# Optimization experiments

Hardware: AMD Instinct MI355X
Metric: run time of the kernel (lower is better)

Reference implementation:

```python
import jax, jax.numpy as jnp
import numpy as np

N = 100000
F = 128
H = 16
C = 40
E = 3200000


def _gcn_norm(edge_index, num_nodes):
    # add self-loops, compute symmetric normalization (PyG GCNConv default)
    loops = jnp.arange(num_nodes, dtype=edge_index.dtype)
    src = jnp.concatenate([edge_index[0], loops])
    dst = jnp.concatenate([edge_index[1], loops])
    ones = jnp.ones(src.shape[0], dtype=jnp.float32)
    deg = jax.ops.segment_sum(ones, dst, num_segments=num_nodes)
    dinv = jnp.where(deg > 0, jax.lax.rsqrt(deg), 0.0)
    norm = dinv[src] * dinv[dst]  # [E+N]
    return src, dst, norm


def _gcn_conv(x, W, b, src, dst, norm, num_nodes):
    h = x @ W                                   # [N, out] transform first (PyG order)
    msg = h[src] * norm[:, None]                # gather + scale
    agg = jax.ops.segment_sum(msg, dst, num_segments=num_nodes)  # scatter-add
    return agg + b


def setup_inputs() -> dict:
    key = jax.random.key(0)
    k = jax.random.split(key, 6)
    x = jax.random.normal(k[0], (N, F), dtype=jnp.float32)
    edge_index = jax.random.randint(k[1], (2, E), 0, N, dtype=jnp.int64)
    W1 = jax.random.normal(k[2], (F, H), dtype=jnp.float32) / np.sqrt(F)
    b1 = jnp.zeros((H,), dtype=jnp.float32)
    W2 = jax.random.normal(k[3], (H, C), dtype=jnp.float32) / np.sqrt(H)
    b2 = jnp.zeros((C,), dtype=jnp.float32)
    return {"x": x, "edge_index": edge_index, "W1": W1, "b1": b1, "W2": W2, "b2": b2}


def reference(x, edge_index, W1, b1, W2, b2):
    src, dst, norm = _gcn_norm(edge_index, N)
    h = _gcn_conv(x, W1, b1, src, dst, norm, N)
    h = jax.nn.relu(h)
    out = _gcn_conv(h, W2, b2, src, dst, norm, N)
    return out
```

## Files before the change

kernel.cpp:

```cpp
#include <hip/hip_runtime.h>
#include <hip/hip_fp16.h>


#define N_NODES 100000
#define F_IN    128
#define H_MID   16
#define C_OUT   40
#define N_EDGES 3200000

#define EC      8192
#define EBLK    391
#define NBUK    782
#define M_HIST  (NBUK * EBLK)
#define NPART   598
#define SRC_MASK 0x1FFFF
#define NSTRIDE 100352
#define CAP_H   5632


__global__ void __launch_bounds__(1024) k_hist(
    const int* __restrict__ dst, int* __restrict__ hist) {
    __shared__ int h[NBUK];
    int t = threadIdx.x, blk = blockIdx.x;
    for (int i = t; i < NBUK; i += 1024) h[i] = 0;
    __syncthreads();
#pragma unroll
    for (int i = 0; i < EC / 1024; ++i) {
        int e = blk * EC + i * 1024 + t;
        if (e < N_EDGES) atomicAdd(&h[__builtin_nontemporal_load(dst + e) >> 7], 1);
    }
    __syncthreads();
    for (int b = t; b < NBUK; b += 1024) hist[b * EBLK + blk] = h[b];
}

__global__ void __launch_bounds__(512) k_scanA(int* __restrict__ hist,
                                               int* __restrict__ part) {
    __shared__ int s[512];
    int t = threadIdx.x;
    int i = blockIdx.x * 512 + t;
    int v = (i < M_HIST) ? hist[i] : 0;
    s[t] = v;
    __syncthreads();
    for (int off = 1; off < 512; off <<= 1) {
        int x = (t >= off) ? s[t - off] : 0;
        __syncthreads();
        s[t] += x;
        __syncthreads();
    }
    if (i < M_HIST) hist[i] = s[t] - v;
    if (t == 511) part[blockIdx.x] = s[511];
}

__global__ void __launch_bounds__(1024) k_scanB(int* __restrict__ part) {
    __shared__ int s[1024];
    int t = threadIdx.x;
    int v = (t < NPART) ? part[t] : 0;
    s[t] = v;
    __syncthreads();
    for (int off = 1; off < 1024; off <<= 1) {
        int x = (t >= off) ? s[t - off] : 0;
        __syncthreads();
        s[t] += x;
        __syncthreads();
    }
    if (t < NPART) part[t] = s[t] - v;
}

__global__ void __launch_bounds__(1024) k_part(
    const int* __restrict__ src, const int* __restrict__ dst,
    const int* __restrict__ hist, const int* __restrict__ part,
    int* __restrict__ eb) {
    __shared__ int cnt[NBUK];
    __shared__ int scn[1024];
    __shared__ int dlt[NBUK];
    __shared__ int cr[NBUK];
    __shared__ int sval[EC];
    __shared__ int spos[EC];
    int t = threadIdx.x, blk = blockIdx.x;
    for (int b = t; b < NBUK; b += 1024) cnt[b] = 0;
    __syncthreads();
    int e0 = blk * EC;
    int d[8], s[8], bk[8];
    bool val[8];
#pragma unroll
    for (int k = 0; k < 8; ++k) {
        int e = e0 + k * 1024 + t;
        val[k] = (e < N_EDGES);
        d[k] = val[k] ? __builtin_nontemporal_load(dst + e) : 0;
        s[k] = val[k] ? __builtin_nontemporal_load(src + e) : 0;
        bk[k] = d[k] >> 7;
    }
#pragma unroll
    for (int k = 0; k < 8; ++k)
        if (val[k]) atomicAdd(&cnt[bk[k]], 1);
    __syncthreads();
    scn[t] = (t < NBUK) ? cnt[t] : 0;
    __syncthreads();
    for (int off = 1; off < 1024; off <<= 1) {
        int x = (t >= off) ? scn[t - off] : 0;
        __syncthreads();
        scn[t] += x;
        __syncthreads();
    }
    for (int b = t; b < NBUK; b += 1024) {
        int idx = b * EBLK + blk;
        int gb = hist[idx] + part[idx >> 9];
        int lb = scn[b] - cnt[b];
        dlt[b] = gb - lb;
        cr[b] = lb;
    }
    __syncthreads();
#pragma unroll
    for (int k = 0; k < 8; ++k) {
        if (val[k]) {
            int lr = atomicAdd(&cr[bk[k]], 1);
            sval[lr] = ((d[k] & 127) << 17) | s[k];
            spos[lr] = lr + dlt[bk[k]];
        }
    }
    __syncthreads();
    int n = (e0 + EC <= N_EDGES) ? EC : (N_EDGES - e0);
    for (int i = t; i < n; i += 1024)
        eb[spos[i]] = sval[i];
}

__global__ void __launch_bounds__(512) k_degrp(
    const int* __restrict__ hist, const int* __restrict__ part,
    const int* __restrict__ eb, int* __restrict__ rp,
    float* __restrict__ dinv) {
    __shared__ int deg[128], scn[128];
    int b = blockIdx.x, t = threadIdx.x;
    int i0 = b * EBLK;
    int bb = hist[i0] + part[i0 >> 9];
    int bn = (b + 1 < NBUK) ? (hist[i0 + EBLK] + part[(i0 + EBLK) >> 9]) : N_EDGES;
    int ecnt = bn - bb;
    if (t < 128) deg[t] = 0;
    __syncthreads();
    for (int i = t; i < ecnt; i += 512)
        atomicAdd(&deg[__builtin_nontemporal_load(eb + bb + i) >> 17], 1);
    __syncthreads();
    if (t < 128) scn[t] = deg[t];
    __syncthreads();
    for (int off = 1; off < 128; off <<= 1) {
        int x = (t < 128 && t >= off) ? scn[t - off] : 0;
        __syncthreads();
        if (t < 128) scn[t] += x;
        __syncthreads();
    }
    if (t < 128) {
        int ex = scn[t] - deg[t];
        int node = b * 128 + t;
        rp[node] = bb + ex;
        dinv[node] = rsqrtf(1.0f + (float)deg[t]);
    }
}


typedef float f4 __attribute__((ext_vector_type(4)));

__global__ void __launch_bounds__(256) k_gemm1(
    const float* __restrict__ x, const float* __restrict__ W1,
    const float* __restrict__ dinv, __half* __restrict__ h1p) {
    __shared__ float w[F_IN * H_MID];
    __shared__ float xs[16 * 132];
    int t = threadIdx.x;
    for (int i = t; i < F_IN * H_MID; i += 256) w[i] = W1[i];
    int tile = blockIdx.x;
    const f4* xg = (const f4*)(x + (size_t)tile * 16 * F_IN);
    f4* xs4 = (f4*)xs;
    for (int i = t; i < 512; i += 256) {
        int r = i >> 5, c4 = i & 31;
        xs4[r * 33 + c4] = __builtin_nontemporal_load(xg + r * 32 + c4);
    }
    __syncthreads();
    int node = t >> 4, j = t & 15;
    const float* xr = xs + node * 132;
    float acc = 0.f;
#pragma unroll 8
    for (int k = 0; k < F_IN; ++k) acc += xr[k] * w[k * H_MID + j];
    int g = tile * 16 + node;
    h1p[(size_t)g * H_MID + j] = __float2half(acc * dinv[g]);
}

__global__ void __launch_bounds__(1024) k_csrg1(
    const int* __restrict__ hist, const int* __restrict__ part,
    const int* __restrict__ eb, const int* __restrict__ rp,
    const float* __restrict__ dinv, const __half* __restrict__ h1p,
    const float* __restrict__ b1, __half* __restrict__ r1p) {
    __shared__ int base[129];
    __shared__ int cw[128];
    __shared__ int esl[CAP_H];
    int b = blockIdx.x, t = threadIdx.x;
    int i0 = b * EBLK;
    int bb = hist[i0] + part[i0 >> 9];
    int bn = (b + 1 < NBUK) ? (hist[i0 + EBLK] + part[(i0 + EBLK) >> 9]) : N_EDGES;
    int ecnt = bn - bb;
    int n0 = b * 128;
    if (t < 128) {
        int lb = rp[n0 + t] - bb;
        base[t] = lb;
        cw[t] = lb;
    }
    if (t == 128) base[128] = ecnt;
    __syncthreads();
    int g = t >> 4, j = t & 15;
    if (ecnt <= CAP_H) {
        for (int i = t; i < ecnt; i += 1024) {
            int v = __builtin_nontemporal_load(eb + bb + i);
            int r = atomicAdd(&cw[v >> 17], 1);
            esl[r] = v & SRC_MASK;
        }
        __syncthreads();
        for (int nd = g; nd < 128; nd += 64) {
            int node = n0 + nd;
            if (node >= N_NODES) continue;
            float dv = dinv[node];
            int beg = base[nd], end = base[nd + 1];
            float acc = __half2float(h1p[(size_t)node * H_MID + j]);
            int e = beg;
            for (; e + 8 <= end; e += 8) {
                int s0 = esl[e],     s1 = esl[e + 1], s2 = esl[e + 2], s3 = esl[e + 3];
                int s4 = esl[e + 4], s5 = esl[e + 5], s6 = esl[e + 6], s7 = esl[e + 7];
                acc += __half2float(h1p[(size_t)s0 * H_MID + j])
                     + __half2float(h1p[(size_t)s1 * H_MID + j])
                     + __half2float(h1p[(size_t)s2 * H_MID + j])
                     + __half2float(h1p[(size_t)s3 * H_MID + j])
                     + __half2float(h1p[(size_t)s4 * H_MID + j])
                     + __half2float(h1p[(size_t)s5 * H_MID + j])
                     + __half2float(h1p[(size_t)s6 * H_MID + j])
                     + __half2float(h1p[(size_t)s7 * H_MID + j]);
            }
            for (; e < end; ++e) acc += __half2float(h1p[(size_t)esl[e] * H_MID + j]);
            float a = dv * acc;
            unsigned short o = __half_as_ushort(__float2half(fmaxf(a + b1[j], 0.f) * dv));
            __builtin_nontemporal_store(o, (unsigned short*)(r1p + (size_t)node * H_MID + j));
        }
    } else {
        for (int nd = g; nd < 128; nd += 64) {
            int node = n0 + nd;
            if (node >= N_NODES) continue;
            float dv = dinv[node];
            float acc = __half2float(h1p[(size_t)node * H_MID + j]);
            for (int i = 0; i < ecnt; ++i) {
                int v = eb[bb + i];
                if ((v >> 17) == nd)
                    acc += __half2float(h1p[(size_t)(v & SRC_MASK) * H_MID + j]);
            }
            float a = dv * acc;
            unsigned short o = __half_as_ushort(__float2half(fmaxf(a + b1[j], 0.f) * dv));
            __builtin_nontemporal_store(o, (unsigned short*)(r1p + (size_t)node * H_MID + j));
        }
    }
}

__global__ void __launch_bounds__(1024) k_csrg2(
    const int* __restrict__ hist, const int* __restrict__ part,
    const int* __restrict__ eb, const int* __restrict__ rp,
    const float* __restrict__ dinv, const __half* __restrict__ r1p,
    const float* __restrict__ W2, const float* __restrict__ b2,
    float* __restrict__ out) {
    __shared__ int base[129];
    __shared__ int cw[128];
    __shared__ int esl[CAP_H];
    __shared__ float a2[128 * 17];
    __shared__ float w2[H_MID * C_OUT];
    __shared__ float b2l[C_OUT];
    int b = blockIdx.x, t = threadIdx.x;
    int i0 = b * EBLK;
    int bb = hist[i0] + part[i0 >> 9];
    int bn = (b + 1 < NBUK) ? (hist[i0 + EBLK] + part[(i0 + EBLK) >> 9]) : N_EDGES;
    int ecnt = bn - bb;
    int n0 = b * 128;
    if (t < H_MID * C_OUT) w2[t] = W2[t];
    if (t >= 1024 - C_OUT) b2l[t - (1024 - C_OUT)] = b2[t - (1024 - C_OUT)];
    if (t < 128) {
        int lb = rp[n0 + t] - bb;
        base[t] = lb;
        cw[t] = lb;
    }
    if (t == 128) base[128] = ecnt;
    __syncthreads();
    int g = t >> 4, j = t & 15;
    if (ecnt <= CAP_H) {
        for (int i = t; i < ecnt; i += 1024) {
            int v = __builtin_nontemporal_load(eb + bb + i);
            int r = atomicAdd(&cw[v >> 17], 1);
            esl[r] = v & SRC_MASK;
        }
        __syncthreads();
        for (int nd = g; nd < 128; nd += 64) {
            int node = n0 + nd;
            float dv = (node < N_NODES) ? dinv[node] : 0.f;
            int beg = base[nd], end = base[nd + 1];
            float acc = (node < N_NODES) ? __half2float(r1p[(size_t)node * H_MID + j]) : 0.f;
            int e = beg;
            for (; e + 8 <= end; e += 8) {
                int s0 = esl[e],     s1 = esl[e + 1], s2 = esl[e + 2], s3 = esl[e + 3];
                int s4 = esl[e + 4], s5 = esl[e + 5], s6 = esl[e + 6], s7 = esl[e + 7];
                acc += __half2float(r1p[(size_t)s0 * H_MID + j])
                     + __half2float(r1p[(size_t)s1 * H_MID + j])
                     + __half2float(r1p[(size_t)s2 * H_MID + j])
                     + __half2float(r1p[(size_t)s3 * H_MID + j])
                     + __half2float(r1p[(size_t)s4 * H_MID + j])
                     + __half2float(r1p[(size_t)s5 * H_MID + j])
                     + __half2float(r1p[(size_t)s6 * H_MID + j])
                     + __half2float(r1p[(size_t)s7 * H_MID + j]);
            }
            for (; e < end; ++e) acc += __half2float(r1p[(size_t)esl[e] * H_MID + j]);
            a2[nd * 17 + j] = dv * acc;
        }
    } else {
        for (int nd = g; nd < 128; nd += 64) {
            int node = n0 + nd;
            float dv = (node < N_NODES) ? dinv[node] : 0.f;
            float acc = (node < N_NODES) ? __half2float(r1p[(size_t)node * H_MID + j]) : 0.f;
            for (int i = 0; i < ecnt; ++i) {
                int v = eb[bb + i];
                if ((v >> 17) == nd)
                    acc += __half2float(r1p[(size_t)(v & SRC_MASK) * H_MID + j]);
            }
            a2[nd * 17 + j] = dv * acc;
        }
    }
    __syncthreads();
    for (int idx = t; idx < 128 * C_OUT; idx += 1024) {
        int nd = idx / C_OUT, c = idx - nd * C_OUT;
        int node = n0 + nd;
        if (node < N_NODES) {
            float s = b2l[c];
#pragma unroll
            for (int jj = 0; jj < H_MID; ++jj) s += a2[nd * 17 + jj] * w2[jj * C_OUT + c];
            __builtin_nontemporal_store(s, &out[(size_t)node * C_OUT + c]);
        }
    }
}

extern "C" void kernel_launch(void* const* d_in, const int* in_sizes, int n_in,
                              void* d_out, int out_size, void* d_ws, size_t ws_size,
                              hipStream_t stream) {
    const float* x  = (const float*)d_in[0];
    const int*   ei = (const int*)d_in[1];
    const float* W1 = (const float*)d_in[2];
    const float* b1 = (const float*)d_in[3];
    const float* W2 = (const float*)d_in[4];
    const float* b2 = (const float*)d_in[5];
    float* out = (float*)d_out;

    const int* src = ei;
    const int* dst = ei + N_EDGES;

    int* rp     = (int*)d_ws;
    float* dinv = (float*)(rp + NSTRIDE);
    __half* h1p = (__half*)(dinv + NSTRIDE);
    __half* r1p = h1p + (size_t)NSTRIDE * H_MID;
    int* eb     = (int*)(r1p + (size_t)NSTRIDE * H_MID);
    int* hist   = eb + N_EDGES;
    int* part   = hist + 306176;

    k_hist <<<EBLK, 1024, 0, stream>>>(dst, hist);
    k_scanA<<<NPART, 512, 0, stream>>>(hist, part);
    k_scanB<<<1, 1024, 0, stream>>>(part);
    k_part <<<EBLK, 1024, 0, stream>>>(src, dst, hist, part, eb);
    k_degrp<<<NBUK, 512, 0, stream>>>(hist, part, eb, rp, dinv);
    k_gemm1<<<N_NODES / 16, 256, 0, stream>>>(x, W1, dinv, h1p);
    k_csrg1<<<NBUK, 1024, 0, stream>>>(hist, part, eb, rp, dinv, h1p, b1, r1p);
    k_csrg2<<<NBUK, 1024, 0, stream>>>(hist, part, eb, rp, dinv, r1p, W2, b2, out);
}
```

Before: 228.5 us.

## Fuse CSR build stages into one cooperative kernel with grid syncs

Replaces the five separate kernels (histogram, two scans, partition, degree/rowptr) with a single cooperative kernel that uses grid-wide syncs between phases. Edge chunks grow to 12800 per block so 250 blocks cover all edges, and each block keeps its dst/src values in registers and its bucket counts in shared memory across phases, so the partition step no longer re-reads edges from global memory. The aim is to remove launch gaps and the redundant reloads. In exchange it relies on all 250 blocks of 1024 threads, with about 100KB of shared memory each, being co-resident, and grid.sync has its own cost.

New measurement: 364.7 us. 1.6x slower.

```diff
diff --git a/kernel.cpp b/kernel.cpp
--- a/kernel.cpp
+++ b/kernel.cpp
@@ -1,5 +1,6 @@
 #include <hip/hip_runtime.h>
 #include <hip/hip_fp16.h>
+#include <hip/hip_cooperative_groups.h>
 
 
 #define N_NODES 100000
@@ -8,150 +9,136 @@
 #define C_OUT   40
 #define N_EDGES 3200000
 
-#define EC      8192
-#define EBLK    391
+#define EC      12800
+#define EBLK    250
+#define KPT     13
 #define NBUK    782
 #define M_HIST  (NBUK * EBLK)
-#define NPART   598
+#define NSEG    191
 #define SRC_MASK 0x1FFFF
 #define NSTRIDE 100352
 #define CAP_H   5632
 
-
-__global__ void __launch_bounds__(1024) k_hist(
-    const int* __restrict__ dst, int* __restrict__ hist) {
-    __shared__ int h[NBUK];
-    int t = threadIdx.x, blk = blockIdx.x;
-    for (int i = t; i < NBUK; i += 1024) h[i] = 0;
-    __syncthreads();
-#pragma unroll
-    for (int i = 0; i < EC / 1024; ++i) {
-        int e = blk * EC + i * 1024 + t;
-        if (e < N_EDGES) atomicAdd(&h[__builtin_nontemporal_load(dst + e) >> 7], 1);
-    }
-    __syncthreads();
-    for (int b = t; b < NBUK; b += 1024) hist[b * EBLK + blk] = h[b];
-}
-
-__global__ void __launch_bounds__(512) k_scanA(int* __restrict__ hist,
-                                               int* __restrict__ part) {
-    __shared__ int s[512];
-    int t = threadIdx.x;
-    int i = blockIdx.x * 512 + t;
-    int v = (i < M_HIST) ? hist[i] : 0;
-    s[t] = v;
-    __syncthreads();
-    for (int off = 1; off < 512; off <<= 1) {
-        int x = (t >= off) ? s[t - off] : 0;
-        __syncthreads();
-        s[t] += x;
-        __syncthreads();
-    }
-    if (i < M_HIST) hist[i] = s[t] - v;
-    if (t == 511) part[blockIdx.x] = s[511];
-}
-
-__global__ void __launch_bounds__(1024) k_scanB(int* __restrict__ part) {
-    __shared__ int s[1024];
-    int t = threadIdx.x;
-    int v = (t < NPART) ? part[t] : 0;
-    s[t] = v;
-    __syncthreads();
-    for (int off = 1; off < 1024; off <<= 1) {
-        int x = (t >= off) ? s[t - off] : 0;
-        __syncthreads();
-        s[t] += x;
-        __syncthreads();
-    }
-    if (t < NPART) part[t] = s[t] - v;
-}
-
-__global__ void __launch_bounds__(1024) k_part(
+namespace cg = cooperative_groups;
+
+
+__global__ void __launch_bounds__(1024) k_build(
     const int* __restrict__ src, const int* __restrict__ dst,
-    const int* __restrict__ hist, const int* __restrict__ part,
-    int* __restrict__ eb) {
+    int* __restrict__ hist, int* __restrict__ part, int* __restrict__ eb,
+    int* __restrict__ rp, float* __restrict__ dinv) {
     __shared__ int cnt[NBUK];
-    __shared__ int scn[1024];
     __shared__ int dlt[NBUK];
     __shared__ int cr[NBUK];
+    __shared__ int lscn[1024];
     __shared__ int sval[EC];
     __shared__ int spos[EC];
+    cg::grid_group grid = cg::this_grid();
     int t = threadIdx.x, blk = blockIdx.x;
+    int e0 = blk * EC;
+
     for (int b = t; b < NBUK; b += 1024) cnt[b] = 0;
     __syncthreads();
-    int e0 = blk * EC;
-    int d[8], s[8], bk[8];
-    bool val[8];
+    int d[KPT], s[KPT];
 #pragma unroll
-    for (int k = 0; k < 8; ++k) {
-        int e = e0 + k * 1024 + t;
-        val[k] = (e < N_EDGES);
-        d[k] = val[k] ? __builtin_nontemporal_load(dst + e) : 0;
-        s[k] = val[k] ? __builtin_nontemporal_load(src + e) : 0;
-        bk[k] = d[k] >> 7;
+    for (int k = 0; k < KPT; ++k) {
+        int off = k * 1024 + t;
+        if (off < EC) {
+            d[k] = __builtin_nontemporal_load(dst + e0 + off);
+            s[k] = __builtin_nontemporal_load(src + e0 + off);
+        } else { d[k] = 0; s[k] = 0; }
     }
 #pragma unroll
-    for (int k = 0; k < 8; ++k)
-        if (val[k]) atomicAdd(&cnt[bk[k]], 1);
-    __syncthreads();
-    scn[t] = (t < NBUK) ? cnt[t] : 0;
+    for (int k = 0; k < KPT; ++k)
+        if (k * 1024 + t < EC) atomicAdd(&cnt[d[k] >> 7], 1);
+    __syncthreads();
+    for (int b = t; b < NBUK; b += 1024) hist[b * EBLK + blk] = cnt[b];
+    grid.sync();
+
+    if (blk < NSEG) {
+        int i = blk * 1024 + t;
+        int v = (i < M_HIST) ? hist[i] : 0;
+        lscn[t] = v;
+        __syncthreads();
+        for (int off = 1; off < 1024; off <<= 1) {
+            int x = (t >= off) ? lscn[t - off] : 0;
+            __syncthreads();
+            lscn[t] += x;
+            __syncthreads();
+        }
+        if (i < M_HIST) hist[i] = lscn[t] - v;
+        if (t == 1023) part[blk] = lscn[1023];
+    }
+    grid.sync();
+
+    if (blk == 0) {
+        int v = (t < NSEG) ? part[t] : 0;
+        lscn[t] = v;
+        __syncthreads();
+        for (int off = 1; off < 1024; off <<= 1) {
+            int x = (t >= off) ? lscn[t - off] : 0;
+            __syncthreads();
+            lscn[t] += x;
+            __syncthreads();
+        }
+        if (t < NSEG) part[t] = lscn[t] - v;
+    }
+    grid.sync();
+
+    lscn[t] = (t < NBUK) ? cnt[t] : 0;
     __syncthreads();
     for (int off = 1; off < 1024; off <<= 1) {
-        int x = (t >= off) ? scn[t - off] : 0;
-        __syncthreads();
-        scn[t] += x;
+        int x = (t >= off) ? lscn[t - off] : 0;
+        __syncthreads();
+        lscn[t] += x;
         __syncthreads();
     }
     for (int b = t; b < NBUK; b += 1024) {
         int idx = b * EBLK + blk;
-        int gb = hist[idx] + part[idx >> 9];
-        int lb = scn[b] - cnt[b];
+        int gb = hist[idx] + part[idx >> 10];
+        int lb = lscn[b] - cnt[b];
         dlt[b] = gb - lb;
         cr[b] = lb;
     }
     __syncthreads();
 #pragma unroll
-    for (int k = 0; k < 8; ++k) {
-        if (val[k]) {
-            int lr = atomicAdd(&cr[bk[k]], 1);
+    for (int k = 0; k < KPT; ++k) {
+        if (k * 1024 + t < EC) {
+            int bk = d[k] >> 7;
+            int lr = atomicAdd(&cr[bk], 1);
             sval[lr] = ((d[k] & 127) << 17) | s[k];
-            spos[lr] = lr + dlt[bk[k]];
-        }
-    }
-    __syncthreads();
-    int n = (e0 + EC <= N_EDGES) ? EC : (N_EDGES - e0);
-    for (int i = t; i < n; i += 1024)
+            spos[lr] = lr + dlt[bk];
+        }
+    }
+    __syncthreads();
+    for (int i = t; i < EC; i += 1024)
         eb[spos[i]] = sval[i];
-}
-
-__global__ void __launch_bounds__(512) k_degrp(
-    const int* __restrict__ hist, const int* __restrict__ part,
-    const int* __restrict__ eb, int* __restrict__ rp,
-    float* __restrict__ dinv) {
-    __shared__ int deg[128], scn[128];
-    int b = blockIdx.x, t = threadIdx.x;
-    int i0 = b * EBLK;
-    int bb = hist[i0] + part[i0 >> 9];
-    int bn = (b + 1 < NBUK) ? (hist[i0 + EBLK] + part[(i0 + EBLK) >> 9]) : N_EDGES;
-    int ecnt = bn - bb;
-    if (t < 128) deg[t] = 0;
-    __syncthreads();
-    for (int i = t; i < ecnt; i += 512)
-        atomicAdd(&deg[__builtin_nontemporal_load(eb + bb + i) >> 17], 1);
-    __syncthreads();
-    if (t < 128) scn[t] = deg[t];
-    __syncthreads();
-    for (int off = 1; off < 128; off <<= 1) {
-        int x = (t < 128 && t >= off) ? scn[t - off] : 0;
-        __syncthreads();
-        if (t < 128) scn[t] += x;
-        __syncthreads();
-    }
-    if (t < 128) {
-        int ex = scn[t] - deg[t];
-        int node = b * 128 + t;
-        rp[node] = bb + ex;
-        dinv[node] = rsqrtf(1.0f + (float)deg[t]);
+    grid.sync();
+
+    for (int b = blk; b < NBUK; b += gridDim.x) {
+        int i0 = b * EBLK;
+        int bb = hist[i0] + part[i0 >> 10];
+        int bn = (b + 1 < NBUK) ? (hist[i0 + EBLK] + part[(i0 + EBLK) >> 10]) : N_EDGES;
+        int ecnt = bn - bb;
+        if (t < 128) cnt[t] = 0;
+        __syncthreads();
+        for (int i = t; i < ecnt; i += 1024)
+            atomicAdd(&cnt[eb[bb + i] >> 17], 1);
+        __syncthreads();
+        if (t < 128) lscn[t] = cnt[t];
+        __syncthreads();
+        for (int off = 1; off < 128; off <<= 1) {
+            int x = (t < 128 && t >= off) ? lscn[t - off] : 0;
+            __syncthreads();
+            if (t < 128) lscn[t] += x;
+            __syncthreads();
+        }
+        if (t < 128) {
+            int ex = lscn[t] - cnt[t];
+            int node = b * 128 + t;
+            rp[node] = bb + ex;
+            dinv[node] = rsqrtf(1.0f + (float)cnt[t]);
+        }
+        __syncthreads();
     }
 }
 
@@ -192,8 +179,8 @@
     __shared__ int esl[CAP_H];
     int b = blockIdx.x, t = threadIdx.x;
     int i0 = b * EBLK;
-    int bb = hist[i0] + part[i0 >> 9];
-    int bn = (b + 1 < NBUK) ? (hist[i0 + EBLK] + part[(i0 + EBLK) >> 9]) : N_EDGES;
+    int bb = hist[i0] + part[i0 >> 10];
+    int bn = (b + 1 < NBUK) ? (hist[i0 + EBLK] + part[(i0 + EBLK) >> 10]) : N_EDGES;
     int ecnt = bn - bb;
     int n0 = b * 128;
     if (t < 128) {
@@ -267,8 +254,8 @@
     __shared__ float b2l[C_OUT];
     int b = blockIdx.x, t = threadIdx.x;
     int i0 = b * EBLK;
-    int bb = hist[i0] + part[i0 >> 9];
-    int bn = (b + 1 < NBUK) ? (hist[i0 + EBLK] + part[(i0 + EBLK) >> 9]) : N_EDGES;
+    int bb = hist[i0] + part[i0 >> 10];
+    int bn = (b + 1 < NBUK) ? (hist[i0 + EBLK] + part[(i0 + EBLK) >> 10]) : N_EDGES;
     int ecnt = bn - bb;
     int n0 = b * 128;
     if (t < H_MID * C_OUT) w2[t] = W2[t];
@@ -355,13 +342,22 @@
     __half* r1p = h1p + (size_t)NSTRIDE * H_MID;
     int* eb     = (int*)(r1p + (size_t)NSTRIDE * H_MID);
     int* hist   = eb + N_EDGES;
-    int* part   = hist + 306176;
-
-    k_hist <<<EBLK, 1024, 0, stream>>>(dst, hist);
-    k_scanA<<<NPART, 512, 0, stream>>>(hist, part);
-    k_scanB<<<1, 1024, 0, stream>>>(part);
-    k_part <<<EBLK, 1024, 0, stream>>>(src, dst, hist, part, eb);
-    k_degrp<<<NBUK, 512, 0, stream>>>(hist, part, eb, rp, dinv);
+    int* part   = hist + 195584;
+
+    {
+        const int* src_a = src;
+        const int* dst_a = dst;
+        int* hist_a = hist;
+        int* part_a = part;
+        int* eb_a = eb;
+        int* rp_a = rp;
+        float* dinv_a = dinv;
+        void* args[] = {(void*)&src_a, (void*)&dst_a, (void*)&hist_a,
+                        (void*)&part_a, (void*)&eb_a, (void*)&rp_a,
+                        (void*)&dinv_a};
+        hipLaunchCooperativeKernel((const void*)k_build, dim3(EBLK), dim3(1024),
+                                   args, 0, stream);
+    }
     k_gemm1<<<N_NODES / 16, 256, 0, stream>>>(x, W1, dinv, h1p);
     k_csrg1<<<NBUK, 1024, 0, stream>>>(hist, part, eb, rp, dinv, h1p, b1, r1p);
     k_csrg2<<<NBUK, 1024, 0, stream>>>(hist, part, eb, rp, dinv, r1p, W2, b2, out);
```

## Co-schedule dense x@W1 with edge histogram; apply dinv scaling in degree kernel

Applied to the files above, without the earlier changes.

Merges the destination histogram and the unscaled x@W1 transform into one launch, with block index choosing the role, so the dense GEMM runs alongside the histogram instead of after degree computation. The unscaled fp32 result goes to the output buffer as scratch. The degree kernel then scales it by dinv and writes the fp16 copy, which removes one kernel launch and one serial dependency. In exchange, the histogram blocks drop from 1024 to 256 threads, and an extra fp32 round trip through memory is added.

Result: no change. 226.0 us (-1.1%).

```diff
diff --git a/kernel.cpp b/kernel.cpp
--- a/kernel.cpp
+++ b/kernel.cpp
@@ -16,21 +16,50 @@
 #define SRC_MASK 0x1FFFF
 #define NSTRIDE 100352
 #define CAP_H   5632
-
-
-__global__ void __launch_bounds__(1024) k_hist(
-    const int* __restrict__ dst, int* __restrict__ hist) {
-    __shared__ int h[NBUK];
+#define GEMM_TILES 6250
+
+typedef float f4 __attribute__((ext_vector_type(4)));
+
+
+__global__ void __launch_bounds__(256) k_histgemm(
+    const int* __restrict__ dst, int* __restrict__ hist,
+    const float* __restrict__ x, const float* __restrict__ W1,
+    float* __restrict__ h1u) {
+    __shared__ __align__(16) char smem[16640];
     int t = threadIdx.x, blk = blockIdx.x;
-    for (int i = t; i < NBUK; i += 1024) h[i] = 0;
-    __syncthreads();
-#pragma unroll
-    for (int i = 0; i < EC / 1024; ++i) {
-        int e = blk * EC + i * 1024 + t;
-        if (e < N_EDGES) atomicAdd(&h[__builtin_nontemporal_load(dst + e) >> 7], 1);
-    }
-    __syncthreads();
-    for (int b = t; b < NBUK; b += 1024) hist[b * EBLK + blk] = h[b];
+    if (blk < EBLK) {
+        int* h = (int*)smem;
+        for (int i = t; i < NBUK; i += 256) h[i] = 0;
+        __syncthreads();
+        int e0 = blk * EC;
+#pragma unroll
+        for (int i = 0; i < EC / 256; ++i) {
+            int e = e0 + i * 256 + t;
+            if (e < N_EDGES)
+                atomicAdd(&h[__builtin_nontemporal_load(dst + e) >> 7], 1);
+        }
+        __syncthreads();
+        for (int b = t; b < NBUK; b += 256) hist[b * EBLK + blk] = h[b];
+    } else {
+        float* w  = (float*)smem;
+        float* xs = (float*)(smem + 8192);
+        int tile = blk - EBLK;
+        for (int i = t; i < F_IN * H_MID; i += 256) w[i] = W1[i];
+        const f4* xg = (const f4*)(x + (size_t)tile * 16 * F_IN);
+        f4* xs4 = (f4*)xs;
+        for (int i = t; i < 512; i += 256) {
+            int r = i >> 5, c4 = i & 31;
+            xs4[r * 33 + c4] = __builtin_nontemporal_load(xg + r * 32 + c4);
+        }
+        __syncthreads();
+        int node = t >> 4, j = t & 15;
+        const float* xr = xs + node * 132;
+        float acc = 0.f;
+#pragma unroll 8
+        for (int k = 0; k < F_IN; ++k) acc += xr[k] * w[k * H_MID + j];
+        int g = tile * 16 + node;
+        h1u[(size_t)g * H_MID + j] = acc;
+    }
 }
 
 __global__ void __launch_bounds__(512) k_scanA(int* __restrict__ hist,
@@ -126,9 +155,10 @@
 
 __global__ void __launch_bounds__(512) k_degrp(
     const int* __restrict__ hist, const int* __restrict__ part,
-    const int* __restrict__ eb, int* __restrict__ rp,
-    float* __restrict__ dinv) {
+    const int* __restrict__ eb, const float* __restrict__ h1u,
+    int* __restrict__ rp, float* __restrict__ dinv, __half* __restrict__ h1p) {
     __shared__ int deg[128], scn[128];
+    __shared__ float sdv[128];
     int b = blockIdx.x, t = threadIdx.x;
     int i0 = b * EBLK;
     int bb = hist[i0] + part[i0 >> 9];
@@ -150,36 +180,21 @@
     if (t < 128) {
         int ex = scn[t] - deg[t];
         int node = b * 128 + t;
+        float dv = rsqrtf(1.0f + (float)deg[t]);
         rp[node] = bb + ex;
-        dinv[node] = rsqrtf(1.0f + (float)deg[t]);
-    }
-}
-
-
-typedef float f4 __attribute__((ext_vector_type(4)));
-
-__global__ void __launch_bounds__(256) k_gemm1(
-    const float* __restrict__ x, const float* __restrict__ W1,
-    const float* __restrict__ dinv, __half* __restrict__ h1p) {
-    __shared__ float w[F_IN * H_MID];
-    __shared__ float xs[16 * 132];
-    int t = threadIdx.x;
-    for (int i = t; i < F_IN * H_MID; i += 256) w[i] = W1[i];
-    int tile = blockIdx.x;
-    const f4* xg = (const f4*)(x + (size_t)tile * 16 * F_IN);
-    f4* xs4 = (f4*)xs;
-    for (int i = t; i < 512; i += 256) {
-        int r = i >> 5, c4 = i & 31;
-        xs4[r * 33 + c4] = __builtin_nontemporal_load(xg + r * 32 + c4);
-    }
-    __syncthreads();
-    int node = t >> 4, j = t & 15;
-    const float* xr = xs + node * 132;
-    float acc = 0.f;
-#pragma unroll 8
-    for (int k = 0; k < F_IN; ++k) acc += xr[k] * w[k * H_MID + j];
-    int g = tile * 16 + node;
-    h1p[(size_t)g * H_MID + j] = __float2half(acc * dinv[g]);
+        dinv[node] = dv;
+        sdv[t] = dv;
+    }
+    __syncthreads();
+    int n0 = b * 128;
+    for (int i = t; i < 128 * H_MID; i += 512) {
+        int node = n0 + (i >> 4);
+        if (node < N_NODES) {
+            float v = h1u[(size_t)n0 * H_MID + i] * sdv[i >> 4];
+            unsigned short o = __half_as_ushort(__float2half(v));
+            __builtin_nontemporal_store(o, (unsigned short*)(h1p + (size_t)n0 * H_MID + i));
+        }
+    }
 }
 
 __global__ void __launch_bounds__(1024) k_csrg1(
@@ -356,13 +371,13 @@
     int* eb     = (int*)(r1p + (size_t)NSTRIDE * H_MID);
     int* hist   = eb + N_EDGES;
     int* part   = hist + 306176;
-
-    k_hist <<<EBLK, 1024, 0, stream>>>(dst, hist);
+    float* h1u  = (float*)d_out;
+
+    k_histgemm<<<EBLK + GEMM_TILES, 256, 0, stream>>>(dst, hist, x, W1, h1u);
     k_scanA<<<NPART, 512, 0, stream>>>(hist, part);
     k_scanB<<<1, 1024, 0, stream>>>(part);
     k_part <<<EBLK, 1024, 0, stream>>>(src, dst, hist, part, eb);
-    k_degrp<<<NBUK, 512, 0, stream>>>(hist, part, eb, rp, dinv);
-    k_gemm1<<<N_NODES / 16, 256, 0, stream>>>(x, W1, dinv, h1p);
+    k_degrp<<<NBUK, 512, 0, stream>>>(hist, part, eb, h1u, rp, dinv, h1p);
     k_csrg1<<<NBUK, 1024, 0, stream>>>(hist, part, eb, rp, dinv, h1p, b1, r1p);
     k_csrg2<<<NBUK, 1024, 0, stream>>>(hist, part, eb, rp, dinv, r1p, W2, b2, out);
 }
```
